# Optimization experiments

Hardware: AMD Instinct MI355X
Metric: run time of the kernel (lower is better)

## Reference

```python
import jax, jax.numpy as jnp
import numpy as np

DIM = 1024
NUM_HEADS = 16
HEAD_DIM = DIM // NUM_HEADS
EPS = 1e-6


def _xavier(key, shape, gain=0.1):
    fan_in, fan_out = shape[1], shape[0]
    limit = gain * np.sqrt(6.0 / (fan_in + fan_out))
    return jax.random.uniform(key, shape, jnp.float32, -limit, limit)


def setup_inputs() -> dict:
    key = jax.random.key(0)
    kx, kq, kk, kv, ko = jax.random.split(key, 5)
    B, N = 4, 4096
    return {
        "x": jax.random.normal(kx, (B, N, DIM), jnp.float32),
        "Wq": _xavier(kq, (DIM, DIM)), "bq": jnp.zeros((DIM,), jnp.float32),
        "Wk": _xavier(kk, (DIM, DIM)), "bk": jnp.zeros((DIM,), jnp.float32),
        "Wv": _xavier(kv, (DIM, DIM)), "bv": jnp.zeros((DIM,), jnp.float32),
        "Wo": _xavier(ko, (DIM, DIM)), "bo": jnp.zeros((DIM,), jnp.float32),
    }


def _phi(x):
    # ELU feature map: elu(x) + 1 ensures non-negativity
    return jax.nn.elu(x) + 1.0


def reference(x, Wq, bq, Wk, bk, Wv, bv, Wo, bo):
    B, N, D = x.shape
    H, Hd = NUM_HEADS, HEAD_DIM
    # torch Linear: y = x @ W.T + b
    Q = (x @ Wq.T + bq).reshape(B, N, H, Hd).transpose(0, 2, 1, 3)
    K = (x @ Wk.T + bk).reshape(B, N, H, Hd).transpose(0, 2, 1, 3)
    V = (x @ Wv.T + bv).reshape(B, N, H, Hd).transpose(0, 2, 1, 3)
    Q = _phi(Q)
    K = _phi(K)
    KV = jnp.einsum('bhnd,bhne->bhde', K, V)          # [B,H,Hd,Hd] state
    out = jnp.einsum('bhnd,bhde->bhne', Q, KV)        # [B,H,N,Hd]
    Z = K.sum(axis=2)                                  # [B,H,Hd]
    norm = jnp.einsum('bhnd,bhd->bhn', Q, Z)[..., None] + EPS
    out = out / norm
    out = out.transpose(0, 2, 1, 3).reshape(B, N, D)
    return out @ Wo.T + bo
```

## Files before the change

### kernel.cpp

```cpp
#include <hip/hip_runtime.h>
#include <math.h>

#define DIMC 1024
#define SEQ 4096
#define BATCH 4
#define NH 16
#define HD 64
#define MTOT (BATCH * SEQ)
#define NSPLIT 8
#define PELEMS (64 * 64 * 64 + 64 * 64)
#define EPS 1e-6f
#define NKT (DIMC / 64)

typedef __bf16 bf16x8 __attribute__((ext_vector_type(8)));
typedef __bf16 bf16x4 __attribute__((ext_vector_type(4)));
typedef __bf16 bf16x2 __attribute__((ext_vector_type(2)));
typedef float  f32x4  __attribute__((ext_vector_type(4)));

#define MFMA16 __builtin_amdgcn_mfma_f32_16x16x32_bf16

__device__ __forceinline__ float phi_f(float x) {
    return x > 0.0f ? x + 1.0f : __expf(x);
}

__global__ __launch_bounds__(256) void cvt_all(
    const float* __restrict__ x,
    const float* __restrict__ Wq, const float* __restrict__ Wk,
    const float* __restrict__ Wv, const float* __restrict__ Wo,
    __bf16* __restrict__ xb,
    __bf16* __restrict__ Wqb, __bf16* __restrict__ Wkb,
    __bf16* __restrict__ Wvb, __bf16* __restrict__ Wob)
{
    const size_t big = (size_t)MTOT * DIMC;
    const size_t wsz = (size_t)DIMC * DIMC;
    size_t i = ((size_t)blockIdx.x * 256 + threadIdx.x) * 4;
    const float* src; __bf16* dst; size_t off;
    if (i < big) { src = x; dst = xb; off = i; }
    else {
        size_t j = i - big;
        int w = (int)(j >> 20);
        off = j & (wsz - 1);
        switch (w) {
            case 0: src = Wq; dst = Wqb; break;
            case 1: src = Wk; dst = Wkb; break;
            case 2: src = Wv; dst = Wvb; break;
            default: src = Wo; dst = Wob; break;
        }
    }
    float4 v = *(const float4*)(src + off);
    bf16x4 o = { (__bf16)v.x, (__bf16)v.y, (__bf16)v.z, (__bf16)v.w };
    *(bf16x4*)(dst + off) = o;
}

template<int OUT_BF16>
__device__ __forceinline__ void gemm_tile256(
    const __bf16* __restrict__ X, const __bf16* __restrict__ W,
    const float* __restrict__ bias, void* __restrict__ Yv,
    int m0, int n0, int do_phi)
{
    __shared__ __attribute__((aligned(16))) __bf16 lds[65536];
    const int tid  = threadIdx.x;
    const int wave = tid >> 6, lane = tid & 63;
    const int wm = wave >> 2, wn = wave & 3;
    const int fr = lane & 15, fkb = lane >> 4;
    const int fsw = fr & 7;
    const int srow = lane >> 3;
    const int sblk = (lane & 7) ^ srow;

    const __bf16* Asrc = X + (size_t)(m0 + wave * 8 + srow) * DIMC + sblk * 8;
    const __bf16* Bsrc = W + (size_t)(n0 + wave * 8 + srow) * DIMC + sblk * 8;
    __bf16* lw = lds + wave * 512;

    auto stage = [&](int isB, int h, int kblk, int bb) {
        const __bf16* s = (isB ? Bsrc : Asrc)
                          + (size_t)(h * 128) * DIMC + (size_t)kblk * 64;
        __bf16* d = lw + bb * 32768 + isB * 16384 + h * 8192;
        #pragma unroll
        for (int g = 0; g < 2; ++g)
            __builtin_amdgcn_global_load_lds(
                (const __attribute__((address_space(1))) void*)(s + (size_t)g * 64 * DIMC),
                (__attribute__((address_space(3))) void*)(d + g * 4096),
                16, 0, 0);
    };
    auto lda = [&](int bb, int i, int ks) -> bf16x8 {
        return *(const bf16x8*)(lds + bb * 32768 + wm * 8192
                 + (i * 16 + fr) * 64 + (((ks * 4 + fkb) ^ fsw) * 8));
    };
    auto ldb = [&](int bb, int j, int ks) -> bf16x8 {
        return *(const bf16x8*)(lds + bb * 32768 + 16384 + (wn >> 1) * 8192
                 + ((wn & 1) * 64 + j * 16 + fr) * 64 + (((ks * 4 + fkb) ^ fsw) * 8));
    };

    f32x4 acc[8][4] = {};
    bf16x8 a[4][2], b[4][2];

    stage(1, 0, 0, 0); stage(1, 1, 0, 0);
    stage(0, 0, 0, 0); stage(0, 1, 0, 0);
    stage(1, 0, 1, 1); stage(1, 1, 1, 1);
    stage(0, 0, 1, 1);
    asm volatile("s_waitcnt vmcnt(6)" ::: "memory");
    __builtin_amdgcn_s_barrier();

    #pragma unroll 2
    for (int t = 0; t < NKT; ++t) {
        const int buf = t & 1;
        #pragma unroll
        for (int i = 0; i < 4; ++i)
            #pragma unroll
            for (int ks = 0; ks < 2; ++ks) a[i][ks] = lda(buf, i, ks);
        #pragma unroll
        for (int j = 0; j < 2; ++j)
            #pragma unroll
            for (int ks = 0; ks < 2; ++ks) b[j][ks] = ldb(buf, j, ks);
        if (t + 1 < NKT) stage(0, 1, t + 1, buf ^ 1);
        __builtin_amdgcn_s_barrier();
        asm volatile("s_waitcnt lgkmcnt(0)" ::: "memory");
        __builtin_amdgcn_s_setprio(1);
        #pragma unroll
        for (int i = 0; i < 4; ++i)
            #pragma unroll
            for (int j = 0; j < 2; ++j)
                #pragma unroll
                for (int ks = 0; ks < 2; ++ks)
                    acc[i][j] = MFMA16(a[i][ks], b[j][ks], acc[i][j], 0, 0, 0);
        __builtin_amdgcn_s_setprio(0);
        __builtin_amdgcn_s_barrier();
        #pragma unroll
        for (int j = 2; j < 4; ++j)
            #pragma unroll
            for (int ks = 0; ks < 2; ++ks) b[j][ks] = ldb(buf, j, ks);
        __builtin_amdgcn_s_barrier();
        asm volatile("s_waitcnt lgkmcnt(0)" ::: "memory");
        __builtin_amdgcn_s_setprio(1);
        #pragma unroll
        for (int i = 0; i < 4; ++i)
            #pragma unroll
            for (int j = 2; j < 4; ++j)
                #pragma unroll
                for (int ks = 0; ks < 2; ++ks)
                    acc[i][j] = MFMA16(a[i][ks], b[j][ks], acc[i][j], 0, 0, 0);
        __builtin_amdgcn_s_setprio(0);
        __builtin_amdgcn_s_barrier();
        #pragma unroll
        for (int i = 0; i < 4; ++i)
            #pragma unroll
            for (int ks = 0; ks < 2; ++ks) a[i][ks] = lda(buf, i + 4, ks);
        if (t + 2 < NKT) stage(1, 0, t + 2, buf);
        __builtin_amdgcn_s_barrier();
        asm volatile("s_waitcnt lgkmcnt(0)" ::: "memory");
        __builtin_amdgcn_s_setprio(1);
        #pragma unroll
        for (int i = 0; i < 4; ++i)
            #pragma unroll
            for (int j = 2; j < 4; ++j)
                #pragma unroll
                for (int ks = 0; ks < 2; ++ks)
                    acc[i + 4][j] = MFMA16(a[i][ks], b[j][ks], acc[i + 4][j], 0, 0, 0);
        __builtin_amdgcn_s_setprio(0);
        __builtin_amdgcn_s_barrier();
        if (t + 2 < NKT) {
            stage(1, 1, t + 2, buf);
            stage(0, 0, t + 2, buf);
        }
        __builtin_amdgcn_s_setprio(1);
        #pragma unroll
        for (int i = 0; i < 4; ++i)
            #pragma unroll
            for (int j = 0; j < 2; ++j)
                #pragma unroll
                for (int ks = 0; ks < 2; ++ks)
                    acc[i + 4][j] = MFMA16(a[i][ks], b[j][ks], acc[i + 4][j], 0, 0, 0);
        __builtin_amdgcn_s_setprio(0);
        if (t < NKT - 2)       asm volatile("s_waitcnt vmcnt(6)" ::: "memory");
        else if (t == NKT - 2) asm volatile("s_waitcnt vmcnt(0)" ::: "memory");
        __builtin_amdgcn_s_barrier();
    }

    const int col_l = lane & 15, quad = lane >> 4;
    const int cbase = n0 + wn * 64 + col_l;
    float bb4[4];
    #pragma unroll
    for (int j = 0; j < 4; ++j) bb4[j] = bias[cbase + j * 16];
    #pragma unroll
    for (int i = 0; i < 8; ++i) {
        #pragma unroll
        for (int r = 0; r < 4; ++r) {
            const size_t grow = (size_t)(m0 + wm * 128 + i * 16 + quad * 4 + r) * DIMC;
            #pragma unroll
            for (int j = 0; j < 4; ++j) {
                float v = acc[i][j][r] + bb4[j];
                if (do_phi) v = phi_f(v);
                if (OUT_BF16)
                    ((__bf16*)Yv)[grow + cbase + j * 16] = (__bf16)v;
                else
                    ((float*)Yv)[grow + cbase + j * 16] = v;
            }
        }
    }
}

__global__ __launch_bounds__(512, 2) void gemm_qkv(
    const __bf16* __restrict__ X,
    const __bf16* __restrict__ Wq, const __bf16* __restrict__ Wk,
    const __bf16* __restrict__ Wv,
    const float* __restrict__ bq, const float* __restrict__ bk,
    const float* __restrict__ bv,
    __bf16* __restrict__ Q, __bf16* __restrict__ K, __bf16* __restrict__ V)
{
    const int l = blockIdx.x;
    const int xcd = l & 7, s = l >> 3;
    const int mat = s >> 5;
    const int t = s & 31;
    const int nb = t & 3;
    const int m_idx = xcd * 8 + (t >> 2);
    const __bf16* W = (mat == 0) ? Wq : (mat == 1) ? Wk : Wv;
    const float* bias = (mat == 0) ? bq : (mat == 1) ? bk : bv;
    __bf16* Y = (mat == 0) ? Q : (mat == 1) ? K : V;
    gemm_tile256<1>(X, W, bias, (void*)Y, m_idx * 256, nb * 256, mat != 2);
}

__global__ __launch_bounds__(512, 2) void gemm_out(
    const __bf16* __restrict__ A, const __bf16* __restrict__ Wo,
    const float* __restrict__ bo, float* __restrict__ out)
{
    const int l = blockIdx.x;
    const int xcd = l & 7, s = l >> 3;
    const int m_idx = xcd * 8 + (s >> 2);
    const int nb = s & 3;
    gemm_tile256<0>(A, Wo, bo, (void*)out, m_idx * 256, nb * 256, 0);
}

__global__ __launch_bounds__(256) void kv_z_kernel(
    const __bf16* __restrict__ Kb, const __bf16* __restrict__ Vb,
    float* __restrict__ P)
{
    __shared__ __attribute__((aligned(16))) __bf16 Kt[2][64 * 36];
    __shared__ __attribute__((aligned(16))) __bf16 Vt[2][64 * 36];
    __shared__ float zs[64];
    const int tid = threadIdx.x, wave = tid >> 6, lane = tid & 63;
    const int bh = blockIdx.x, b = bh >> 4, h = bh & 15;
    const int split = blockIdx.y;
    const int n0 = split * (SEQ / NSPLIT);
    const int dg = (tid & 15) * 4;
    const int u2 = (tid >> 4) * 2;
    const int fr = lane & 15, fk = (lane >> 4) * 8;
    const __bf16* Kp = Kb + ((size_t)b * SEQ + n0) * DIMC + h * HD;
    const __bf16* Vp = Vb + ((size_t)b * SEQ + n0) * DIMC + h * HD;
    constexpr int CH = (SEQ / NSPLIT) / 32;

    if (tid < 64) zs[tid] = 0.0f;
    f32x4 acc[4] = {};
    float zp[4] = {};

    auto ldc = [&](int c, bf16x4& ka, bf16x4& kb, bf16x4& va, bf16x4& vb) {
        ka = *(const bf16x4*)(Kp + (size_t)(c * 32 + u2) * DIMC + dg);
        kb = *(const bf16x4*)(Kp + (size_t)(c * 32 + u2 + 1) * DIMC + dg);
        va = *(const bf16x4*)(Vp + (size_t)(c * 32 + u2) * DIMC + dg);
        vb = *(const bf16x4*)(Vp + (size_t)(c * 32 + u2 + 1) * DIMC + dg);
    };

    bf16x4 ka, kb, va, vb;
    ldc(0, ka, kb, va, vb);

    for (int c = 0; c < CH; ++c) {
        const int p = c & 1;
        #pragma unroll
        for (int q = 0; q < 4; ++q) {
            zp[q] += (float)ka[q] + (float)kb[q];
            *(bf16x2*)(Kt[p] + (dg + q) * 36 + u2) = bf16x2{ka[q], kb[q]};
            *(bf16x2*)(Vt[p] + (dg + q) * 36 + u2) = bf16x2{va[q], vb[q]};
        }
        bf16x4 nka, nkb, nva, nvb;
        if (c + 1 < CH) ldc(c + 1, nka, nkb, nva, nvb);
        __syncthreads();

        const __bf16* ar = Kt[p] + (wave * 16 + fr) * 36 + fk;
        bf16x4 alo = *(const bf16x4*)ar, ahi = *(const bf16x4*)(ar + 4);
        bf16x8 af = {alo[0],alo[1],alo[2],alo[3],ahi[0],ahi[1],ahi[2],ahi[3]};
        #pragma unroll
        for (int j = 0; j < 4; ++j) {
            const __bf16* br = Vt[p] + (j * 16 + fr) * 36 + fk;
            bf16x4 blo = *(const bf16x4*)br, bhi = *(const bf16x4*)(br + 4);
            bf16x8 bf = {blo[0],blo[1],blo[2],blo[3],bhi[0],bhi[1],bhi[2],bhi[3]};
            acc[j] = __builtin_amdgcn_mfma_f32_16x16x32_bf16(af, bf, acc[j], 0, 0, 0);
        }
        ka = nka; kb = nkb; va = nva; vb = nvb;
    }

    #pragma unroll
    for (int q = 0; q < 4; ++q) atomicAdd(&zs[dg + q], zp[q]);
    __syncthreads();

    float* KVp = P + (size_t)split * PELEMS + bh * 4096;
    const int col_l = lane & 15, quad = lane >> 4;
    #pragma unroll
    for (int j = 0; j < 4; ++j)
        #pragma unroll
        for (int r = 0; r < 4; ++r)
            KVp[(wave * 16 + quad * 4 + r) * 64 + j * 16 + col_l] = acc[j][r];
    if (tid < 64)
        P[(size_t)split * PELEMS + 64 * 64 * 64 + bh * 64 + tid] = zs[tid];
}

__global__ __launch_bounds__(256) void reduce_partials(
    const float* __restrict__ P, float* __restrict__ F)
{
    const int i = blockIdx.x * 256 + threadIdx.x;
    if (i < PELEMS) {
        float s = 0.0f;
        #pragma unroll
        for (int sp = 0; sp < NSPLIT; ++sp) s += P[(size_t)sp * PELEMS + i];
        F[i] = s;
    }
}

__global__ __launch_bounds__(256) void attn_apply(
    const __bf16* __restrict__ Qb, const float* __restrict__ F,
    __bf16* __restrict__ Ab)
{
    __shared__ __align__(16) float  Ftmp[4096];
    __shared__ __align__(16) __bf16 KVhi[64 * 80];
    __shared__ __align__(16) __bf16 KVlo[64 * 80];
    __shared__ __align__(16) __bf16 Qs[128 * 80];
    const int tid = threadIdx.x, wave = tid >> 6, lane = tid & 63;
    const int bhh = blockIdx.y, b = bhh >> 4, h = bhh & 15;
    const int n0 = blockIdx.x * 128;

    const float* KVp = F + (size_t)bhh * 4096;
    #pragma unroll
    for (int r = 0; r < 4; ++r) {
        const int idx = (r * 256 + tid) * 4;
        *(float4*)&Ftmp[idx] = *(const float4*)(KVp + idx);
    }
    const __bf16* Qp = Qb + ((size_t)(b * SEQ + n0)) * DIMC + h * HD;
    const int qrow = tid >> 3, qcol = (tid & 7) * 8;
    bf16x8 qv[4];
    #pragma unroll
    for (int rr = 0; rr < 4; ++rr)
        qv[rr] = *(const bf16x8*)(Qp + (size_t)(rr * 32 + qrow) * DIMC + qcol);
    __syncthreads();

    {
        const int e = tid >> 2, d0 = (tid & 3) * 16;
        #pragma unroll
        for (int k = 0; k < 16; k += 2) {
            float v0 = Ftmp[(d0 + k) * 64 + e];
            float v1 = Ftmp[(d0 + k + 1) * 64 + e];
            __bf16 h0 = (__bf16)v0, h1 = (__bf16)v1;
            *(bf16x2*)(KVhi + e * 80 + d0 + k) = bf16x2{h0, h1};
            *(bf16x2*)(KVlo + e * 80 + d0 + k) =
                bf16x2{(__bf16)(v0 - (float)h0), (__bf16)(v1 - (float)h1)};
        }
        #pragma unroll
        for (int rr = 0; rr < 4; ++rr)
            *(bf16x8*)(Qs + (rr * 32 + qrow) * 80 + qcol) = qv[rr];
    }
    __syncthreads();

    const int tt = lane & 31, half = lane >> 5;
    float part = 0.0f;
    const float* Zp = F + 64 * 64 * 64 + bhh * HD + half * 32;
    #pragma unroll
    for (int g = 0; g < 4; ++g) {
        bf16x8 q8 = *(const bf16x8*)(Qs + (wave * 32 + tt) * 80 + half * 32 + g * 8);
        float4 z0 = *(const float4*)(Zp + g * 8);
        float4 z1 = *(const float4*)(Zp + g * 8 + 4);
        part = fmaf((float)q8[0], z0.x, part);
        part = fmaf((float)q8[1], z0.y, part);
        part = fmaf((float)q8[2], z0.z, part);
        part = fmaf((float)q8[3], z0.w, part);
        part = fmaf((float)q8[4], z1.x, part);
        part = fmaf((float)q8[5], z1.y, part);
        part = fmaf((float)q8[6], z1.z, part);
        part = fmaf((float)q8[7], z1.w, part);
    }
    part += __shfl_xor(part, 32);
    const float rn = 1.0f / (part + EPS);

    const int fr = lane & 15, fkb = lane >> 4;
    f32x4 acc[2][4] = {};
    #pragma unroll
    for (int ks = 0; ks < 2; ++ks) {
        bf16x8 a0 = *(const bf16x8*)(Qs + (wave * 32 + fr) * 80 + ks * 32 + fkb * 8);
        bf16x8 a1 = *(const bf16x8*)(Qs + (wave * 32 + 16 + fr) * 80 + ks * 32 + fkb * 8);
        #pragma unroll
        for (int j = 0; j < 4; ++j) {
            bf16x8 bh8 = *(const bf16x8*)(KVhi + (j * 16 + fr) * 80 + ks * 32 + fkb * 8);
            bf16x8 bl8 = *(const bf16x8*)(KVlo + (j * 16 + fr) * 80 + ks * 32 + fkb * 8);
            acc[0][j] = MFMA16(a0, bh8, acc[0][j], 0, 0, 0);
            acc[0][j] = MFMA16(a0, bl8, acc[0][j], 0, 0, 0);
            acc[1][j] = MFMA16(a1, bh8, acc[1][j], 0, 0, 0);
            acc[1][j] = MFMA16(a1, bl8, acc[1][j], 0, 0, 0);
        }
    }

    const int col_l = lane & 15, quad = lane >> 4;
    #pragma unroll
    for (int i = 0; i < 2; ++i) {
        #pragma unroll
        for (int r = 0; r < 4; ++r) {
            const float rni = __shfl(rn, i * 16 + quad * 4 + r);
            const int tok = n0 + wave * 32 + i * 16 + quad * 4 + r;
            __bf16* Op = Ab + ((size_t)(b * SEQ + tok)) * DIMC + h * HD + col_l;
            #pragma unroll
            for (int j = 0; j < 4; ++j)
                Op[j * 16] = (__bf16)(acc[i][j][r] * rni);
        }
    }
}

extern "C" void kernel_launch(void* const* d_in, const int* in_sizes, int n_in,
                              void* d_out, int out_size, void* d_ws, size_t ws_size,
                              hipStream_t stream) {
    const float* x  = (const float*)d_in[0];
    const float* Wq = (const float*)d_in[1];
    const float* bq = (const float*)d_in[2];
    const float* Wk = (const float*)d_in[3];
    const float* bk = (const float*)d_in[4];
    const float* Wv = (const float*)d_in[5];
    const float* bv = (const float*)d_in[6];
    const float* Wo = (const float*)d_in[7];
    const float* bo = (const float*)d_in[8];
    float* out = (float*)d_out;

    const size_t big = (size_t)MTOT * DIMC;
    const size_t wsz = (size_t)DIMC * DIMC;
    __bf16* wsp = (__bf16*)d_ws;
    __bf16* xb  = wsp;
    __bf16* Wqb = xb + big;
    __bf16* Wkb = Wqb + wsz;
    __bf16* Wvb = Wkb + wsz;
    __bf16* Wob = Wvb + wsz;
    __bf16* Qb  = Wob + wsz;
    __bf16* Kb  = Qb + big;
    __bf16* Vb  = Kb + big;
    __bf16* Ab  = xb;
    float*  P   = (float*)(Vb + big);
    float*  F   = P + (size_t)NSPLIT * PELEMS;

    const size_t ntot = big + 4 * wsz;
    cvt_all<<<dim3((int)(ntot / 1024)), 256, 0, stream>>>(
        x, Wq, Wk, Wv, Wo, xb, Wqb, Wkb, Wvb, Wob);

    gemm_qkv<<<dim3(768), 512, 0, stream>>>(
        xb, Wqb, Wkb, Wvb, bq, bk, bv, Qb, Kb, Vb);

    kv_z_kernel<<<dim3(BATCH * NH, NSPLIT), 256, 0, stream>>>(Kb, Vb, P);
    reduce_partials<<<dim3((PELEMS + 255) / 256), 256, 0, stream>>>(P, F);
    attn_apply<<<dim3(SEQ / 128, BATCH * NH), 256, 0, stream>>>(Qb, F, Ab);

    gemm_out<<<dim3(256), 512, 0, stream>>>(Ab, Wob, bo, out);
}
```

Measured before the change: 302.2 us.

## Switch GEMM tile to 32x32x16 MFMA and widen conversion per thread

Replaces the 16x16x32 bf16 MFMA fragments in the shared GEMM tile routine with 32x32x16 MFMAs. LDS fragment addressing, the accumulator layout and the epilogue store mapping are reworked to match. This halves the number of MFMA issues and reduces LDS fragment reads per FLOP. Separately, the fp32-to-bf16 conversion kernel now handles 16 elements per thread with a quarter of the blocks, cutting launch and index overhead. The risks are a different register footprint and a less coalesced epilogue store pattern.

```diff
diff --git a/kernel.cpp b/kernel.cpp
--- a/kernel.cpp
+++ b/kernel.cpp
@@ -16,8 +16,10 @@
 typedef __bf16 bf16x4 __attribute__((ext_vector_type(4)));
 typedef __bf16 bf16x2 __attribute__((ext_vector_type(2)));
 typedef float  f32x4  __attribute__((ext_vector_type(4)));
+typedef float  f32x16 __attribute__((ext_vector_type(16)));
 
 #define MFMA16 __builtin_amdgcn_mfma_f32_16x16x32_bf16
+#define MFMA32 __builtin_amdgcn_mfma_f32_32x32x16_bf16
 
 __device__ __forceinline__ float phi_f(float x) {
     return x > 0.0f ? x + 1.0f : __expf(x);
@@ -33,7 +35,7 @@
 {
     const size_t big = (size_t)MTOT * DIMC;
     const size_t wsz = (size_t)DIMC * DIMC;
-    size_t i = ((size_t)blockIdx.x * 256 + threadIdx.x) * 4;
+    size_t i = ((size_t)blockIdx.x * 256 + threadIdx.x) * 16;
     const float* src; __bf16* dst; size_t off;
     if (i < big) { src = x; dst = xb; off = i; }
     else {
@@ -47,9 +49,12 @@
             default: src = Wo; dst = Wob; break;
         }
     }
-    float4 v = *(const float4*)(src + off);
-    bf16x4 o = { (__bf16)v.x, (__bf16)v.y, (__bf16)v.z, (__bf16)v.w };
-    *(bf16x4*)(dst + off) = o;
+    #pragma unroll
+    for (int g = 0; g < 4; ++g) {
+        float4 v = *(const float4*)(src + off + g * 4);
+        bf16x4 o = { (__bf16)v.x, (__bf16)v.y, (__bf16)v.z, (__bf16)v.w };
+        *(bf16x4*)(dst + off + g * 4) = o;
+    }
 }
 
 template<int OUT_BF16>
@@ -62,8 +67,8 @@
     const int tid  = threadIdx.x;
     const int wave = tid >> 6, lane = tid & 63;
     const int wm = wave >> 2, wn = wave & 3;
-    const int fr = lane & 15, fkb = lane >> 4;
-    const int fsw = fr & 7;
+    const int r32 = lane & 31, khalf = lane >> 5;
+    const int fsw = r32 & 7;
     const int srow = lane >> 3;
     const int sblk = (lane & 7) ^ srow;
 
@@ -82,17 +87,17 @@
                 (__attribute__((address_space(3))) void*)(d + g * 4096),
                 16, 0, 0);
     };
-    auto lda = [&](int bb, int i, int ks) -> bf16x8 {
+    auto lda = [&](int bb, int i, int s) -> bf16x8 {
         return *(const bf16x8*)(lds + bb * 32768 + wm * 8192
-                 + (i * 16 + fr) * 64 + (((ks * 4 + fkb) ^ fsw) * 8));
+                 + (i * 32 + r32) * 64 + (((s * 2 + khalf) ^ fsw) * 8));
     };
-    auto ldb = [&](int bb, int j, int ks) -> bf16x8 {
+    auto ldb = [&](int bb, int j, int s) -> bf16x8 {
         return *(const bf16x8*)(lds + bb * 32768 + 16384 + (wn >> 1) * 8192
-                 + ((wn & 1) * 64 + j * 16 + fr) * 64 + (((ks * 4 + fkb) ^ fsw) * 8));
+                 + ((wn & 1) * 64 + j * 32 + r32) * 64 + (((s * 2 + khalf) ^ fsw) * 8));
     };
 
-    f32x4 acc[8][4] = {};
-    bf16x8 a[4][2], b[4][2];
+    f32x16 acc[4][2] = {};
+    bf16x8 a[2][4], b[2][4];
 
     stage(1, 0, 0, 0); stage(1, 1, 0, 0);
     stage(0, 0, 0, 0); stage(0, 1, 0, 0);
@@ -105,57 +110,47 @@
     for (int t = 0; t < NKT; ++t) {
         const int buf = t & 1;
         #pragma unroll
-        for (int i = 0; i < 4; ++i)
-            #pragma unroll
-            for (int ks = 0; ks < 2; ++ks) a[i][ks] = lda(buf, i, ks);
-        #pragma unroll
-        for (int j = 0; j < 2; ++j)
-            #pragma unroll
-            for (int ks = 0; ks < 2; ++ks) b[j][ks] = ldb(buf, j, ks);
+        for (int i = 0; i < 2; ++i)
+            #pragma unroll
+            for (int s = 0; s < 4; ++s) a[i][s] = lda(buf, i, s);
+        #pragma unroll
+        for (int s = 0; s < 4; ++s) b[0][s] = ldb(buf, 0, s);
         if (t + 1 < NKT) stage(0, 1, t + 1, buf ^ 1);
         __builtin_amdgcn_s_barrier();
         asm volatile("s_waitcnt lgkmcnt(0)" ::: "memory");
         __builtin_amdgcn_s_setprio(1);
         #pragma unroll
-        for (int i = 0; i < 4; ++i)
-            #pragma unroll
-            for (int j = 0; j < 2; ++j)
-                #pragma unroll
-                for (int ks = 0; ks < 2; ++ks)
-                    acc[i][j] = MFMA16(a[i][ks], b[j][ks], acc[i][j], 0, 0, 0);
+        for (int i = 0; i < 2; ++i)
+            #pragma unroll
+            for (int s = 0; s < 4; ++s)
+                acc[i][0] = MFMA32(a[i][s], b[0][s], acc[i][0], 0, 0, 0);
         __builtin_amdgcn_s_setprio(0);
         __builtin_amdgcn_s_barrier();
         #pragma unroll
-        for (int j = 2; j < 4; ++j)
-            #pragma unroll
-            for (int ks = 0; ks < 2; ++ks) b[j][ks] = ldb(buf, j, ks);
+        for (int s = 0; s < 4; ++s) b[1][s] = ldb(buf, 1, s);
         __builtin_amdgcn_s_barrier();
         asm volatile("s_waitcnt lgkmcnt(0)" ::: "memory");
         __builtin_amdgcn_s_setprio(1);
         #pragma unroll
-        for (int i = 0; i < 4; ++i)
-            #pragma unroll
-            for (int j = 2; j < 4; ++j)
-                #pragma unroll
-                for (int ks = 0; ks < 2; ++ks)
-                    acc[i][j] = MFMA16(a[i][ks], b[j][ks], acc[i][j], 0, 0, 0);
+        for (int i = 0; i < 2; ++i)
+            #pragma unroll
+            for (int s = 0; s < 4; ++s)
+                acc[i][1] = MFMA32(a[i][s], b[1][s], acc[i][1], 0, 0, 0);
         __builtin_amdgcn_s_setprio(0);
         __builtin_amdgcn_s_barrier();
         #pragma unroll
-        for (int i = 0; i < 4; ++i)
-            #pragma unroll
-            for (int ks = 0; ks < 2; ++ks) a[i][ks] = lda(buf, i + 4, ks);
+        for (int i = 0; i < 2; ++i)
+            #pragma unroll
+            for (int s = 0; s < 4; ++s) a[i][s] = lda(buf, i + 2, s);
         if (t + 2 < NKT) stage(1, 0, t + 2, buf);
         __builtin_amdgcn_s_barrier();
         asm volatile("s_waitcnt lgkmcnt(0)" ::: "memory");
         __builtin_amdgcn_s_setprio(1);
         #pragma unroll
-        for (int i = 0; i < 4; ++i)
-            #pragma unroll
-            for (int j = 2; j < 4; ++j)
-                #pragma unroll
-                for (int ks = 0; ks < 2; ++ks)
-                    acc[i + 4][j] = MFMA16(a[i][ks], b[j][ks], acc[i + 4][j], 0, 0, 0);
+        for (int i = 0; i < 2; ++i)
+            #pragma unroll
+            for (int s = 0; s < 4; ++s)
+                acc[i + 2][1] = MFMA32(a[i][s], b[1][s], acc[i + 2][1], 0, 0, 0);
         __builtin_amdgcn_s_setprio(0);
         __builtin_amdgcn_s_barrier();
         if (t + 2 < NKT) {
@@ -164,36 +159,35 @@
         }
         __builtin_amdgcn_s_setprio(1);
         #pragma unroll
-        for (int i = 0; i < 4; ++i)
-            #pragma unroll
-            for (int j = 0; j < 2; ++j)
-                #pragma unroll
-                for (int ks = 0; ks < 2; ++ks)
-                    acc[i + 4][j] = MFMA16(a[i][ks], b[j][ks], acc[i + 4][j], 0, 0, 0);
+        for (int i = 0; i < 2; ++i)
+            #pragma unroll
+            for (int s = 0; s < 4; ++s)
+                acc[i + 2][0] = MFMA32(a[i][s], b[0][s], acc[i + 2][0], 0, 0, 0);
         __builtin_amdgcn_s_setprio(0);
         if (t < NKT - 2)       asm volatile("s_waitcnt vmcnt(6)" ::: "memory");
         else if (t == NKT - 2) asm volatile("s_waitcnt vmcnt(0)" ::: "memory");
         __builtin_amdgcn_s_barrier();
     }
 
-    const int col_l = lane & 15, quad = lane >> 4;
-    const int cbase = n0 + wn * 64 + col_l;
-    float bb4[4];
-    #pragma unroll
-    for (int j = 0; j < 4; ++j) bb4[j] = bias[cbase + j * 16];
-    #pragma unroll
-    for (int i = 0; i < 8; ++i) {
-        #pragma unroll
-        for (int r = 0; r < 4; ++r) {
-            const size_t grow = (size_t)(m0 + wm * 128 + i * 16 + quad * 4 + r) * DIMC;
-            #pragma unroll
-            for (int j = 0; j < 4; ++j) {
-                float v = acc[i][j][r] + bb4[j];
-                if (do_phi) v = phi_f(v);
-                if (OUT_BF16)
-                    ((__bf16*)Yv)[grow + cbase + j * 16] = (__bf16)v;
-                else
-                    ((float*)Yv)[grow + cbase + j * 16] = v;
+    float bb2[2];
+    #pragma unroll
+    for (int j = 0; j < 2; ++j) bb2[j] = bias[n0 + wn * 64 + j * 32 + r32];
+    #pragma unroll
+    for (int i = 0; i < 4; ++i) {
+        #pragma unroll
+        for (int rg = 0; rg < 4; ++rg) {
+            #pragma unroll
+            for (int rr = 0; rr < 4; ++rr) {
+                const int row = m0 + wm * 128 + i * 32 + rg * 8 + khalf * 4 + rr;
+                const size_t grow = (size_t)row * DIMC;
+                #pragma unroll
+                for (int j = 0; j < 2; ++j) {
+                    float v = acc[i][j][rg * 4 + rr] + bb2[j];
+                    if (do_phi) v = phi_f(v);
+                    const size_t gi = grow + n0 + wn * 64 + j * 32 + r32;
+                    if (OUT_BF16) ((__bf16*)Yv)[gi] = (__bf16)v;
+                    else          ((float*)Yv)[gi] = v;
+                }
             }
         }
     }
@@ -439,7 +433,7 @@
     float*  F   = P + (size_t)NSPLIT * PELEMS;
 
     const size_t ntot = big + 4 * wsz;
-    cvt_all<<<dim3((int)(ntot / 1024)), 256, 0, stream>>>(
+    cvt_all<<<dim3((int)(ntot / 4096)), 256, 0, stream>>>(
         x, Wq, Wk, Wv, Wo, xb, Wqb, Wkb, Wvb, Wob);
 
     gemm_qkv<<<dim3(768), 512, 0, stream>>>(
```

After: 322.4 us. +6.7%, slower.
